# Kernel optimization log

Measured on AMD Instinct MI355X. Metric: run time of the kernel, lower is better.

Reference implementation:

```python
import jax, jax.numpy as jnp
import numpy as np

N = 8192          # num_relations
IN_DIM = 512      # 2 * entity_dim
HID = 256         # hidden_dim
REL_DIM = 256     # relation_dim


def setup_inputs() -> dict:
    key = jax.random.key(0)
    ks = jax.random.split(key, 8)
    s = 1.0 / np.sqrt(IN_DIM)
    return {
        "relation": jax.random.normal(ks[0], (N, REL_DIM), dtype=jnp.float32),
        "context": jax.random.normal(ks[1], (N, IN_DIM), dtype=jnp.float32),
        "adj_tensor": jax.random.randint(ks[2], (N, N), 0, 2).astype(jnp.float32),
        "W_common": jax.random.normal(ks[3], (HID, IN_DIM), dtype=jnp.float32) * s,
        "w_left": jax.random.normal(ks[4], (HID,), dtype=jnp.float32) * (1.0 / np.sqrt(HID)),
        "b_left": jax.random.normal(ks[5], (), dtype=jnp.float32) * 0.01,
        "w_right": jax.random.normal(ks[6], (HID,), dtype=jnp.float32) * (1.0 / np.sqrt(HID)),
        "b_right": jax.random.normal(ks[7], (), dtype=jnp.float32) * 0.01,
    }


def reference(relation, context, adj_tensor, W_common, w_left, b_left, w_right, b_right):
    # common linear (no bias): (N, IN_DIM) @ (IN_DIM, HID) -> (N, HID)
    in_fts = context @ W_common.T
    left = in_fts @ w_left + b_left          # (N,)
    right = in_fts @ w_right + b_right       # (N,)
    logits = left[:, None] + right[None, :]  # additive outer-sum -> (N, N)
    logits = jnp.where(logits >= 0, logits, 0.2 * logits)  # leaky_relu(0.2)
    logits = jnp.where(adj_tensor <= 0.0, -jnp.inf, logits)
    coefs = jax.nn.softmax(logits, axis=-1)  # (N, N)
    x = coefs @ relation                     # (N, REL_DIM)
    return jax.nn.relu(x)
```

## Files before the change

### kernel.cpp

```cpp
#include <hip/hip_runtime.h>

#define NREL 8192
#define RD   256
#define RSHIFT 16.0f

typedef float f32x4 __attribute__((ext_vector_type(4)));
typedef short s16x8 __attribute__((ext_vector_type(8)));
typedef unsigned int  u32;
typedef unsigned short u16;
typedef unsigned long long u64;
typedef u32 u32x4 __attribute__((ext_vector_type(4)));

__device__ __forceinline__ u16 f2bf(float f) {
    u32 b = __float_as_uint(f);
    return (u16)((b + 0x7FFFu + ((b >> 16) & 1u)) >> 16);
}
__device__ __forceinline__ u32 pk_bf16(float lo, float hi) {
    u32 r;
    asm("v_cvt_pk_bf16_f32 %0, %1, %2" : "=v"(r) : "v"(lo), "v"(hi));
    return r;
}

__global__ __launch_bounds__(256) void k_prep_bf(
    const float* __restrict__ W, const float* __restrict__ wl,
    const float* __restrict__ wr, float* __restrict__ ul,
    float* __restrict__ ur, const float* __restrict__ R,
    u32* __restrict__ Bf)
{
    __shared__ float sL[256], sR[256];
    const int t = threadIdx.x;
    if (blockIdx.x < 32) {
        const int d = blockIdx.x * 16 + (t & 15);
        float aL = 0.f, aR = 0.f;
        for (int h = (t >> 4); h < 256; h += 16) {
            float w = W[h * 512 + d];
            aL += w * wl[h];
            aR += w * wr[h];
        }
        sL[t] = aL; sR[t] = aR;
        __syncthreads();
        if (t < 16) {
            float xL = 0.f, xR = 0.f;
            for (int g = 0; g < 16; g++) { xL += sL[g * 16 + t]; xR += sR[g * 16 + t]; }
            ul[blockIdx.x * 16 + t] = xL;
            ur[blockIdx.x * 16 + t] = xR;
        }
        return;
    }
    if (!Bf) return;
    const int b     = blockIdx.x - 32;
    const int jt    = b >> 1;
    const int fbase = (b & 1) * 1024;
    #pragma unroll
    for (int rep = 0; rep < 4; rep++) {
        const int f    = fbase + rep * 256 + t;
        const int kk   = f >> 10;
        const int cg   = (f >> 6) & 15;
        const int lane = f & 63;
        const int lq   = lane >> 4;
        const int l15  = lane & 15;
        const int j0   = (jt << 6) + kk * 32 + lq * 8;
        const int n    = cg * 16 + l15;
        const float* src = R + (size_t)j0 * RD + n;
        float v[8];
        #pragma unroll
        for (int e = 0; e < 8; e++) v[e] = src[(size_t)e * RD];
        u32x4 w;
        w.x = pk_bf16(v[0], v[1]);
        w.y = pk_bf16(v[2], v[3]);
        w.z = pk_bf16(v[4], v[5]);
        w.w = pk_bf16(v[6], v[7]);
        *(u32x4*)(Bf + ((size_t)jt * 2048 + f) * 4) = w;
    }
}

__global__ __launch_bounds__(256) void k_lr(
    const float* __restrict__ ctx, const float* __restrict__ ul,
    const float* __restrict__ ur, const float* __restrict__ bl,
    const float* __restrict__ br, float* __restrict__ left,
    float* __restrict__ right)
{
    const int lane = threadIdx.x & 63;
    const int row  = blockIdx.x * 4 + (threadIdx.x >> 6);
    const f32x4* cv = (const f32x4*)(ctx + (size_t)row * 512);
    const f32x4* uv = (const f32x4*)ul;
    const f32x4* vv = (const f32x4*)ur;
    f32x4 c0 = cv[lane], c1 = cv[lane + 64];
    f32x4 u0 = uv[lane], u1 = uv[lane + 64];
    f32x4 v0 = vv[lane], v1 = vv[lane + 64];
    float dl = c0.x*u0.x + c0.y*u0.y + c0.z*u0.z + c0.w*u0.w
             + c1.x*u1.x + c1.y*u1.y + c1.z*u1.z + c1.w*u1.w;
    float dr = c0.x*v0.x + c0.y*v0.y + c0.z*v0.z + c0.w*v0.w
             + c1.x*v1.x + c1.y*v1.y + c1.z*v1.z + c1.w*v1.w;
    #pragma unroll
    for (int o = 1; o < 64; o <<= 1) { dl += __shfl_xor(dl, o); dr += __shfl_xor(dr, o); }
    if (lane == 0) {
        left[row]  = dl + bl[0];
        right[row] = dr + br[0];
    }
}

template<int S>
__global__ __launch_bounds__(1024) void k_attn_f(
    const float* __restrict__ adj, const s16x8* __restrict__ Bf,
    const float* __restrict__ left, const float* __restrict__ right,
    float* __restrict__ pnum, float* __restrict__ pden)
{
    __shared__ u32 Pl[2][4096];

    const int tid  = threadIdx.x;
    const int lane = tid & 63;
    const int wv   = tid >> 6;
    const int l15  = lane & 15;
    const int lq   = lane >> 4;
    const int rg   = wv >> 3;
    const int cg8  = wv & 7;
    const int s      = (int)(blockIdx.x % (unsigned)S);
    const int rowblk = (int)(blockIdx.x / (unsigned)S) * 128;
    const int jt0 = s * (128 / S);
    const int jt1 = jt0 + (128 / S);

    const int pr = tid >> 4;
    const int pq = tid & 15;

    const float lft0 = left[rowblk + pr];
    const float lft1 = left[rowblk + pr + 64];
    float z;
    z = lft0 + RSHIFT; const float m0 = fmaxf(z, 0.2f * z);
    z = lft1 + RSHIFT; const float m1 = fmaxf(z, 0.2f * z);

    f32x4 acc[4][2];
    #pragma unroll
    for (int i = 0; i < 4; i++) { acc[i][0] = (f32x4)0.f; acc[i][1] = (f32x4)0.f; }
    float dp0 = 0.f, dp1 = 0.f;

    const f32x4* adjv = (const f32x4*)adj;
    const f32x4* rv4  = (const f32x4*)right;
    const size_t arow0 = (size_t)(rowblk + pr) * 2048;
    const size_t arow1 = (size_t)(rowblk + pr + 64) * 2048;

    const u32 widx0 = (u32)pr * 32 + (((u32)pq * 2) ^ (((u32)pr & 7) << 2));
    const u32 widx1 = widx0 + 2048;

    f32x4 aA0 = adjv[arow0 + jt0 * 16 + pq];
    f32x4 aA1 = adjv[arow1 + jt0 * 16 + pq];
    f32x4 rvA = rv4[jt0 * 16 + pq];
    f32x4 aB0 = adjv[arow0 + (jt0 + 1) * 16 + pq];
    f32x4 aB1 = adjv[arow1 + (jt0 + 1) * 16 + pq];
    f32x4 rvB = rv4[(jt0 + 1) * 16 + pq];
    s16x8 bA[2][2], bB[2][2];
    #pragma unroll
    for (int kk = 0; kk < 2; kk++)
        #pragma unroll
        for (int ct = 0; ct < 2; ct++)
            bA[kk][ct] = Bf[(size_t)jt0 * 2048 + kk * 1024 + (cg8 * 2 + ct) * 64 + lane];

    for (int jt = jt0; jt < jt1; jt += 2) {
        {
            float pa[4], pb[4];
            #pragma unroll
            for (int e = 0; e < 4; e++) {
                const float r = rvA[e];
                float z0 = lft0 + r; float s0 = fmaxf(z0, 0.2f * z0);
                pa[e] = aA0[e] * __expf(s0 - m0);
                float z1 = lft1 + r; float s1 = fmaxf(z1, 0.2f * z1);
                pb[e] = aA1[e] * __expf(s1 - m1);
            }
            dp0 += pa[0] + pa[1] + pa[2] + pa[3];
            dp1 += pb[0] + pb[1] + pb[2] + pb[3];
            Pl[0][widx0]     = pk_bf16(pa[0], pa[1]);
            Pl[0][widx0 + 1] = pk_bf16(pa[2], pa[3]);
            Pl[0][widx1]     = pk_bf16(pb[0], pb[1]);
            Pl[0][widx1 + 1] = pk_bf16(pb[2], pb[3]);

            asm volatile("s_waitcnt lgkmcnt(0)" ::: "memory");
            __builtin_amdgcn_s_barrier();

            const int j2 = (jt + 2 < jt1) ? jt + 2 : jt0;
            aA0 = adjv[arow0 + j2 * 16 + pq];
            aA1 = adjv[arow1 + j2 * 16 + pq];
            rvA = rv4[j2 * 16 + pq];
            #pragma unroll
            for (int kk = 0; kk < 2; kk++)
                #pragma unroll
                for (int ct = 0; ct < 2; ct++)
                    bB[kk][ct] = Bf[(size_t)(jt + 1) * 2048 + kk * 1024
                                    + (cg8 * 2 + ct) * 64 + lane];

            const u16* Pu = (const u16*)Pl[0];
            #pragma unroll
            for (int kk = 0; kk < 2; kk++) {
                s16x8 af[4];
                #pragma unroll
                for (int rt = 0; rt < 4; rt++) {
                    const int row = rg * 64 + rt * 16 + l15;
                    const int us  = row * 64 + ((kk * 32 + lq * 8) ^ ((row & 7) << 3));
                    af[rt] = *(const s16x8*)(Pu + us);
                }
                #pragma unroll
                for (int ct = 0; ct < 2; ct++)
                    #pragma unroll
                    for (int rt = 0; rt < 4; rt++)
                        acc[rt][ct] = __builtin_amdgcn_mfma_f32_16x16x32_bf16(
                            af[rt], bA[kk][ct], acc[rt][ct], 0, 0, 0);
            }
        }
        {
            float pa[4], pb[4];
            #pragma unroll
            for (int e = 0; e < 4; e++) {
                const float r = rvB[e];
                float z0 = lft0 + r; float s0 = fmaxf(z0, 0.2f * z0);
                pa[e] = aB0[e] * __expf(s0 - m0);
                float z1 = lft1 + r; float s1 = fmaxf(z1, 0.2f * z1);
                pb[e] = aB1[e] * __expf(s1 - m1);
            }
            dp0 += pa[0] + pa[1] + pa[2] + pa[3];
            dp1 += pb[0] + pb[1] + pb[2] + pb[3];
            Pl[1][widx0]     = pk_bf16(pa[0], pa[1]);
            Pl[1][widx0 + 1] = pk_bf16(pa[2], pa[3]);
            Pl[1][widx1]     = pk_bf16(pb[0], pb[1]);
            Pl[1][widx1 + 1] = pk_bf16(pb[2], pb[3]);

            asm volatile("s_waitcnt lgkmcnt(0)" ::: "memory");
            __builtin_amdgcn_s_barrier();

            const int j3 = (jt + 3 < jt1) ? jt + 3 : jt0;
            aB0 = adjv[arow0 + j3 * 16 + pq];
            aB1 = adjv[arow1 + j3 * 16 + pq];
            rvB = rv4[j3 * 16 + pq];
            const int j2 = (jt + 2 < jt1) ? jt + 2 : jt0;
            #pragma unroll
            for (int kk = 0; kk < 2; kk++)
                #pragma unroll
                for (int ct = 0; ct < 2; ct++)
                    bA[kk][ct] = Bf[(size_t)j2 * 2048 + kk * 1024
                                    + (cg8 * 2 + ct) * 64 + lane];

            const u16* Pu = (const u16*)Pl[1];
            #pragma unroll
            for (int kk = 0; kk < 2; kk++) {
                s16x8 af[4];
                #pragma unroll
                for (int rt = 0; rt < 4; rt++) {
                    const int row = rg * 64 + rt * 16 + l15;
                    const int us  = row * 64 + ((kk * 32 + lq * 8) ^ ((row & 7) << 3));
                    af[rt] = *(const s16x8*)(Pu + us);
                }
                #pragma unroll
                for (int ct = 0; ct < 2; ct++)
                    #pragma unroll
                    for (int rt = 0; rt < 4; rt++)
                        acc[rt][ct] = __builtin_amdgcn_mfma_f32_16x16x32_bf16(
                            af[rt], bB[kk][ct], acc[rt][ct], 0, 0, 0);
            }
        }
    }

    #pragma unroll
    for (int o = 1; o < 16; o <<= 1) { dp0 += __shfl_xor(dp0, o); dp1 += __shfl_xor(dp1, o); }
    if (pq == 0) {
        pden[(size_t)s * NREL + rowblk + pr]      = dp0;
        pden[(size_t)s * NREL + rowblk + pr + 64] = dp1;
    }
    float* pn = pnum + (size_t)s * NREL * RD;
    #pragma unroll
    for (int rt = 0; rt < 4; rt++)
        #pragma unroll
        for (int ct = 0; ct < 2; ct++)
            #pragma unroll
            for (int r = 0; r < 4; r++) {
                const int row = rg * 64 + rt * 16 + lq * 4 + r;
                pn[(size_t)(rowblk + row) * RD + (cg8 * 32 + ct * 16 + l15)] =
                    acc[rt][ct][r];
            }
}

template<int S>
__global__ __launch_bounds__(256) void k_red(
    const float* __restrict__ pnum, const float* __restrict__ pden,
    float* __restrict__ out)
{
    const int idx = blockIdx.x * 256 + threadIdx.x;
    const int row = idx >> 6;
    float den = 0.f;
    #pragma unroll
    for (int s = 0; s < S; s++) den += pden[(size_t)s * NREL + row];
    const f32x4* pn4 = (const f32x4*)pnum;
    f32x4 a = (f32x4)0.f;
    #pragma unroll
    for (int s = 0; s < S; s++) a += pn4[(size_t)s * (NREL * RD / 4) + idx];
    f32x4 r;
    r.x = fmaxf(a.x / den, 0.f);
    r.y = fmaxf(a.y / den, 0.f);
    r.z = fmaxf(a.z / den, 0.f);
    r.w = fmaxf(a.w / den, 0.f);
    ((f32x4*)out)[idx] = r;
}

__global__ __launch_bounds__(512) void k_attn_leg(
    const float* __restrict__ adj, const float* __restrict__ rel,
    const float* __restrict__ left, const float* __restrict__ right,
    float* __restrict__ outp)
{
    __shared__ u32   Pl[64 * 32];
    __shared__ float dnm[64];
    const int tid  = threadIdx.x;
    const int lane = tid & 63;
    const int wv   = tid >> 6;
    const int l15  = lane & 15;
    const int lq   = lane >> 4;
    const int rowblk = blockIdx.x * 64;
    const int pr = tid >> 4, pq = tid & 15;
    const float lft0 = left[rowblk + pr];
    const float lft1 = left[rowblk + pr + 32];
    float z;
    z = lft0 + RSHIFT; const float m0 = fmaxf(z, 0.2f * z);
    z = lft1 + RSHIFT; const float m1 = fmaxf(z, 0.2f * z);
    f32x4 acc[4][2];
    #pragma unroll
    for (int i = 0; i < 4; i++) { acc[i][0] = (f32x4)0.f; acc[i][1] = (f32x4)0.f; }
    float dp0 = 0.f, dp1 = 0.f;
    const f32x4* adjv = (const f32x4*)adj;
    const f32x4* rv4  = (const f32x4*)right;
    const size_t arow0 = (size_t)(rowblk + pr) * 2048;
    const size_t arow1 = (size_t)(rowblk + pr + 32) * 2048;
    const int n0 = wv * 32 + l15;
    const u32 widx0 = (u32)pr * 32 + (((u32)pq * 2) ^ (((u32)pr & 7) << 2));
    const u32 widx1 = widx0 + 1024;
    for (int jb = 0; jb < NREL; jb += 64) {
        f32x4 a0 = adjv[arow0 + (jb >> 2) + pq];
        f32x4 a1 = adjv[arow1 + (jb >> 2) + pq];
        f32x4 rv = rv4[(jb >> 2) + pq];
        s16x8 bc[2][2];
        #pragma unroll
        for (int kk = 0; kk < 2; kk++)
            #pragma unroll
            for (int ct = 0; ct < 2; ct++) {
                const float* rp = rel + (size_t)(jb + kk * 32 + lq * 8) * RD
                                      + (n0 + ct * 16);
                s16x8 b;
                #pragma unroll
                for (int e = 0; e < 8; e++) b[e] = (short)f2bf(rp[(size_t)e * RD]);
                bc[kk][ct] = b;
            }
        float pa[4], pb[4];
        #pragma unroll
        for (int e = 0; e < 4; e++) {
            const float r = rv[e];
            float z0 = lft0 + r; float s0 = fmaxf(z0, 0.2f * z0);
            pa[e] = a0[e] * __expf(s0 - m0);
            float z1 = lft1 + r; float s1 = fmaxf(z1, 0.2f * z1);
            pb[e] = a1[e] * __expf(s1 - m1);
        }
        dp0 += pa[0] + pa[1] + pa[2] + pa[3];
        dp1 += pb[0] + pb[1] + pb[2] + pb[3];
        Pl[widx0]     = pk_bf16(pa[0], pa[1]);
        Pl[widx0 + 1] = pk_bf16(pa[2], pa[3]);
        Pl[widx1]     = pk_bf16(pb[0], pb[1]);
        Pl[widx1 + 1] = pk_bf16(pb[2], pb[3]);
        __syncthreads();
        #pragma unroll
        for (int kk = 0; kk < 2; kk++) {
            s16x8 af[4];
            #pragma unroll
            for (int rt = 0; rt < 4; rt++) {
                const int row = rt * 16 + l15;
                const int us  = row * 64 + ((kk * 32 + lq * 8) ^ ((row & 7) << 3));
                af[rt] = *(const s16x8*)((const u16*)Pl + us);
            }
            #pragma unroll
            for (int ct = 0; ct < 2; ct++)
                #pragma unroll
                for (int rt = 0; rt < 4; rt++)
                    acc[rt][ct] = __builtin_amdgcn_mfma_f32_16x16x32_bf16(
                        af[rt], bc[kk][ct], acc[rt][ct], 0, 0, 0);
        }
        __syncthreads();
    }
    #pragma unroll
    for (int o = 1; o < 16; o <<= 1) { dp0 += __shfl_xor(dp0, o); dp1 += __shfl_xor(dp1, o); }
    if (pq == 0) { dnm[pr] = dp0; dnm[pr + 32] = dp1; }
    __syncthreads();
    #pragma unroll
    for (int rt = 0; rt < 4; rt++)
        #pragma unroll
        for (int ct = 0; ct < 2; ct++)
            #pragma unroll
            for (int r = 0; r < 4; r++) {
                const int row = rt * 16 + lq * 4 + r;
                float v = acc[rt][ct][r] / dnm[row];
                outp[(size_t)(rowblk + row) * RD + (wv * 32 + ct * 16 + l15)] =
                    fmaxf(v, 0.f);
            }
}

extern "C" void kernel_launch(void* const* d_in, const int* in_sizes, int n_in,
                              void* d_out, int out_size, void* d_ws, size_t ws_size,
                              hipStream_t stream)
{
    const float* relation = (const float*)d_in[0];
    const float* context  = (const float*)d_in[1];
    const float* adj      = (const float*)d_in[2];
    const float* W        = (const float*)d_in[3];
    const float* wl       = (const float*)d_in[4];
    const float* bl       = (const float*)d_in[5];
    const float* wr       = (const float*)d_in[6];
    const float* br       = (const float*)d_in[7];
    float* out = (float*)d_out;

    float* wsf   = (float*)d_ws;
    float* ul    = wsf;
    float* ur    = wsf + 512;
    float* left  = wsf + 1024;
    float* right = wsf + 1024 + 8192;
    const size_t hdr  = 81920;
    const size_t bf_b = (size_t)NREL * RD * 2;
    u32* Bf   = (u32*)((char*)d_ws + hdr);
    float* pnum = (float*)((char*)d_ws + hdr + bf_b);

    const int S = 4;
    const size_t need = hdr + bf_b
                      + (size_t)S * NREL * RD * 4 + (size_t)S * NREL * 4;

    if (ws_size >= need) {
        float* pden = pnum + (size_t)S * NREL * RD;
        hipLaunchKernelGGL(k_prep_bf, dim3(288), dim3(256), 0, stream,
                           W, wl, wr, ul, ur, relation, Bf);
        hipLaunchKernelGGL(k_lr, dim3(2048), dim3(256), 0, stream,
                           context, ul, ur, bl, br, left, right);
        hipLaunchKernelGGL((k_attn_f<4>), dim3(64 * 4), dim3(1024), 0, stream,
                           adj, (const s16x8*)Bf, left, right, pnum, pden);
        hipLaunchKernelGGL((k_red<4>), dim3(2048), dim3(256), 0, stream,
                           pnum, pden, out);
    } else {
        hipLaunchKernelGGL(k_prep_bf, dim3(32), dim3(256), 0, stream,
                           W, wl, wr, ul, ur, relation, (u32*)nullptr);
        hipLaunchKernelGGL(k_lr, dim3(2048), dim3(256), 0, stream,
                           context, ul, ur, bl, br, left, right);
        hipLaunchKernelGGL(k_attn_leg, dim3(128), dim3(512), 0, stream,
                           adj, relation, left, right, out);
    }
}
```

Before: 110.4 us.

## Restructure attention kernel to 64-row blocks with 4-tile groups per barrier

The fused attention kernel now uses 512-thread blocks covering 64 rows instead of 1024 threads covering 128, doubling the grid. Each iteration stages four 64-column P tiles in shared memory, with one pair of barriers per group instead of one per tile. Each thread loads 16 contiguous floats of adj per row rather than 4 strided ones. A per-block rotation staggers the starting column group so concurrent blocks read different parts of B. The aim is fewer barriers, wider adjacency loads and better occupancy, at the cost of more registers per thread and B fragments being reused across only 64 rows.

```diff
diff --git a/kernel.cpp b/kernel.cpp
--- a/kernel.cpp
+++ b/kernel.cpp
@@ -101,30 +101,30 @@
 }
 
 template<int S>
-__global__ __launch_bounds__(1024) void k_attn_f(
+__global__ __launch_bounds__(512) void k_attn_f(
     const float* __restrict__ adj, const s16x8* __restrict__ Bf,
     const float* __restrict__ left, const float* __restrict__ right,
     float* __restrict__ pnum, float* __restrict__ pden)
 {
-    __shared__ u32 Pl[2][4096];
+    __shared__ u32 Pt[4 * 2048];
+    constexpr int NT = 128 / S;
+    constexpr int NG = NT / 4;
 
     const int tid  = threadIdx.x;
     const int lane = tid & 63;
     const int wv   = tid >> 6;
     const int l15  = lane & 15;
     const int lq   = lane >> 4;
-    const int rg   = wv >> 3;
-    const int cg8  = wv & 7;
     const int s      = (int)(blockIdx.x % (unsigned)S);
-    const int rowblk = (int)(blockIdx.x / (unsigned)S) * 128;
-    const int jt0 = s * (128 / S);
-    const int jt1 = jt0 + (128 / S);
+    const int rowblk = (int)(blockIdx.x / (unsigned)S) * 64;
+    const int jt0 = s * NT;
+    const int rot = (int)(blockIdx.x & (NG - 1));
 
     const int pr = tid >> 4;
     const int pq = tid & 15;
 
     const float lft0 = left[rowblk + pr];
-    const float lft1 = left[rowblk + pr + 64];
+    const float lft1 = left[rowblk + pr + 32];
     float z;
     z = lft0 + RSHIFT; const float m0 = fmaxf(z, 0.2f * z);
     z = lft1 + RSHIFT; const float m1 = fmaxf(z, 0.2f * z);
@@ -137,131 +137,113 @@
     const f32x4* adjv = (const f32x4*)adj;
     const f32x4* rv4  = (const f32x4*)right;
     const size_t arow0 = (size_t)(rowblk + pr) * 2048;
-    const size_t arow1 = (size_t)(rowblk + pr + 64) * 2048;
-
-    const u32 widx0 = (u32)pr * 32 + (((u32)pq * 2) ^ (((u32)pr & 7) << 2));
-    const u32 widx1 = widx0 + 2048;
-
-    f32x4 aA0 = adjv[arow0 + jt0 * 16 + pq];
-    f32x4 aA1 = adjv[arow1 + jt0 * 16 + pq];
-    f32x4 rvA = rv4[jt0 * 16 + pq];
-    f32x4 aB0 = adjv[arow0 + (jt0 + 1) * 16 + pq];
-    f32x4 aB1 = adjv[arow1 + (jt0 + 1) * 16 + pq];
-    f32x4 rvB = rv4[(jt0 + 1) * 16 + pq];
+    const size_t arow1 = (size_t)(rowblk + pr + 32) * 2048;
+
+    const u32 bc  = (u32)(pq & 3) * 8;
+    const u32 swz = ((u32)pr & 7) << 2;
+    u32* const Pb = Pt + (size_t)(pq >> 2) * 2048;
+
+    #define GBASE(g) (jt0 + (((g) + rot) & (NG - 1)) * 4)
+
+    f32x4 a0[4], a1[4], rr[4];
+    {
+        const int jg = GBASE(0);
+        #pragma unroll
+        for (int q = 0; q < 4; q++) {
+            a0[q] = adjv[arow0 + jg * 16 + pq * 4 + q];
+            a1[q] = adjv[arow1 + jg * 16 + pq * 4 + q];
+            rr[q] = rv4[jg * 16 + pq * 4 + q];
+        }
+    }
     s16x8 bA[2][2], bB[2][2];
     #pragma unroll
     for (int kk = 0; kk < 2; kk++)
         #pragma unroll
         for (int ct = 0; ct < 2; ct++)
-            bA[kk][ct] = Bf[(size_t)jt0 * 2048 + kk * 1024 + (cg8 * 2 + ct) * 64 + lane];
-
-    for (int jt = jt0; jt < jt1; jt += 2) {
-        {
+            bA[kk][ct] = Bf[(size_t)GBASE(0) * 2048 + kk * 1024
+                            + (wv * 2 + ct) * 64 + lane];
+
+    #define BLOAD(DST, JT)                                                     \
+        _Pragma("unroll")                                                      \
+        for (int kk = 0; kk < 2; kk++)                                         \
+            _Pragma("unroll")                                                  \
+            for (int ct = 0; ct < 2; ct++)                                     \
+                DST[kk][ct] = Bf[(size_t)(JT) * 2048 + kk * 1024               \
+                                 + (wv * 2 + ct) * 64 + lane];
+
+    #define MFMA_TILE(TT, BSLOT)                                               \
+        {                                                                      \
+            const u16* Pu = (const u16*)(Pt + (TT) * 2048);                    \
+            _Pragma("unroll")                                                  \
+            for (int kk = 0; kk < 2; kk++) {                                   \
+                s16x8 af[4];                                                   \
+                _Pragma("unroll")                                              \
+                for (int rt = 0; rt < 4; rt++) {                               \
+                    const int row = rt * 16 + l15;                             \
+                    const int us  = row * 64                                   \
+                                  + ((kk * 32 + lq * 8) ^ ((row & 7) << 3));   \
+                    af[rt] = *(const s16x8*)(Pu + us);                         \
+                }                                                              \
+                _Pragma("unroll")                                              \
+                for (int ct = 0; ct < 2; ct++)                                 \
+                    _Pragma("unroll")                                          \
+                    for (int rt = 0; rt < 4; rt++)                             \
+                        acc[rt][ct] = __builtin_amdgcn_mfma_f32_16x16x32_bf16( \
+                            af[rt], BSLOT[kk][ct], acc[rt][ct], 0, 0, 0);      \
+            }                                                                  \
+        }
+
+    for (int g = 0; g < NG; g++) {
+        const int jgc = GBASE(g);
+        const int jgn = GBASE((g + 1 < NG) ? g + 1 : 0);
+
+        #pragma unroll
+        for (int q = 0; q < 4; q++) {
             float pa[4], pb[4];
             #pragma unroll
             for (int e = 0; e < 4; e++) {
-                const float r = rvA[e];
+                const float r = rr[q][e];
                 float z0 = lft0 + r; float s0 = fmaxf(z0, 0.2f * z0);
-                pa[e] = aA0[e] * __expf(s0 - m0);
+                pa[e] = a0[q][e] * __expf(s0 - m0);
                 float z1 = lft1 + r; float s1 = fmaxf(z1, 0.2f * z1);
-                pb[e] = aA1[e] * __expf(s1 - m1);
+                pb[e] = a1[q][e] * __expf(s1 - m1);
             }
             dp0 += pa[0] + pa[1] + pa[2] + pa[3];
             dp1 += pb[0] + pb[1] + pb[2] + pb[3];
-            Pl[0][widx0]     = pk_bf16(pa[0], pa[1]);
-            Pl[0][widx0 + 1] = pk_bf16(pa[2], pa[3]);
-            Pl[0][widx1]     = pk_bf16(pb[0], pb[1]);
-            Pl[0][widx1 + 1] = pk_bf16(pb[2], pb[3]);
-
-            asm volatile("s_waitcnt lgkmcnt(0)" ::: "memory");
-            __builtin_amdgcn_s_barrier();
-
-            const int j2 = (jt + 2 < jt1) ? jt + 2 : jt0;
-            aA0 = adjv[arow0 + j2 * 16 + pq];
-            aA1 = adjv[arow1 + j2 * 16 + pq];
-            rvA = rv4[j2 * 16 + pq];
-            #pragma unroll
-            for (int kk = 0; kk < 2; kk++)
-                #pragma unroll
-                for (int ct = 0; ct < 2; ct++)
-                    bB[kk][ct] = Bf[(size_t)(jt + 1) * 2048 + kk * 1024
-                                    + (cg8 * 2 + ct) * 64 + lane];
-
-            const u16* Pu = (const u16*)Pl[0];
-            #pragma unroll
-            for (int kk = 0; kk < 2; kk++) {
-                s16x8 af[4];
-                #pragma unroll
-                for (int rt = 0; rt < 4; rt++) {
-                    const int row = rg * 64 + rt * 16 + l15;
-                    const int us  = row * 64 + ((kk * 32 + lq * 8) ^ ((row & 7) << 3));
-                    af[rt] = *(const s16x8*)(Pu + us);
-                }
-                #pragma unroll
-                for (int ct = 0; ct < 2; ct++)
-                    #pragma unroll
-                    for (int rt = 0; rt < 4; rt++)
-                        acc[rt][ct] = __builtin_amdgcn_mfma_f32_16x16x32_bf16(
-                            af[rt], bA[kk][ct], acc[rt][ct], 0, 0, 0);
-            }
-        }
-        {
-            float pa[4], pb[4];
-            #pragma unroll
-            for (int e = 0; e < 4; e++) {
-                const float r = rvB[e];
-                float z0 = lft0 + r; float s0 = fmaxf(z0, 0.2f * z0);
-                pa[e] = aB0[e] * __expf(s0 - m0);
-                float z1 = lft1 + r; float s1 = fmaxf(z1, 0.2f * z1);
-                pb[e] = aB1[e] * __expf(s1 - m1);
-            }
-            dp0 += pa[0] + pa[1] + pa[2] + pa[3];
-            dp1 += pb[0] + pb[1] + pb[2] + pb[3];
-            Pl[1][widx0]     = pk_bf16(pa[0], pa[1]);
-            Pl[1][widx0 + 1] = pk_bf16(pa[2], pa[3]);
-            Pl[1][widx1]     = pk_bf16(pb[0], pb[1]);
-            Pl[1][widx1 + 1] = pk_bf16(pb[2], pb[3]);
-
-            asm volatile("s_waitcnt lgkmcnt(0)" ::: "memory");
-            __builtin_amdgcn_s_barrier();
-
-            const int j3 = (jt + 3 < jt1) ? jt + 3 : jt0;
-            aB0 = adjv[arow0 + j3 * 16 + pq];
-            aB1 = adjv[arow1 + j3 * 16 + pq];
-            rvB = rv4[j3 * 16 + pq];
-            const int j2 = (jt + 2 < jt1) ? jt + 2 : jt0;
-            #pragma unroll
-            for (int kk = 0; kk < 2; kk++)
-                #pragma unroll
-                for (int ct = 0; ct < 2; ct++)
-                    bA[kk][ct] = Bf[(size_t)j2 * 2048 + kk * 1024
-                                    + (cg8 * 2 + ct) * 64 + lane];
-
-            const u16* Pu = (const u16*)Pl[1];
-            #pragma unroll
-            for (int kk = 0; kk < 2; kk++) {
-                s16x8 af[4];
-                #pragma unroll
-                for (int rt = 0; rt < 4; rt++) {
-                    const int row = rg * 64 + rt * 16 + l15;
-                    const int us  = row * 64 + ((kk * 32 + lq * 8) ^ ((row & 7) << 3));
-                    af[rt] = *(const s16x8*)(Pu + us);
-                }
-                #pragma unroll
-                for (int ct = 0; ct < 2; ct++)
-                    #pragma unroll
-                    for (int rt = 0; rt < 4; rt++)
-                        acc[rt][ct] = __builtin_amdgcn_mfma_f32_16x16x32_bf16(
-                            af[rt], bB[kk][ct], acc[rt][ct], 0, 0, 0);
-            }
-        }
-    }
+            const u32 i0 = (u32)pr * 32 + ((bc + q * 2) ^ swz);
+            Pb[i0]        = pk_bf16(pa[0], pa[1]);
+            Pb[i0 + 1]    = pk_bf16(pa[2], pa[3]);
+            Pb[i0 + 1024] = pk_bf16(pb[0], pb[1]);
+            Pb[i0 + 1025] = pk_bf16(pb[2], pb[3]);
+        }
+
+        asm volatile("s_waitcnt lgkmcnt(0)" ::: "memory");
+        __builtin_amdgcn_s_barrier();
+
+        #pragma unroll
+        for (int q = 0; q < 4; q++) {
+            a0[q] = adjv[arow0 + jgn * 16 + pq * 4 + q];
+            a1[q] = adjv[arow1 + jgn * 16 + pq * 4 + q];
+            rr[q] = rv4[jgn * 16 + pq * 4 + q];
+        }
+
+        BLOAD(bB, jgc + 1);  MFMA_TILE(0, bA);
+        BLOAD(bA, jgc + 2);  MFMA_TILE(1, bB);
+        BLOAD(bB, jgc + 3);  MFMA_TILE(2, bA);
+        BLOAD(bA, jgn);      MFMA_TILE(3, bB);
+
+        asm volatile("s_waitcnt lgkmcnt(0)" ::: "memory");
+        __builtin_amdgcn_s_barrier();
+    }
+    #undef GBASE
+    #undef BLOAD
+    #undef MFMA_TILE
 
     #pragma unroll
     for (int o = 1; o < 16; o <<= 1) { dp0 += __shfl_xor(dp0, o); dp1 += __shfl_xor(dp1, o); }
     if (pq == 0) {
         pden[(size_t)s * NREL + rowblk + pr]      = dp0;
-        pden[(size_t)s * NREL + rowblk + pr + 64] = dp1;
+        pden[(size_t)s * NREL + rowblk + pr + 32] = dp1;
     }
     float* pn = pnum + (size_t)s * NREL * RD;
     #pragma unroll
@@ -270,8 +252,8 @@
         for (int ct = 0; ct < 2; ct++)
             #pragma unroll
             for (int r = 0; r < 4; r++) {
-                const int row = rg * 64 + rt * 16 + lq * 4 + r;
-                pn[(size_t)(rowblk + row) * RD + (cg8 * 32 + ct * 16 + l15)] =
+                const int row = rt * 16 + lq * 4 + r;
+                pn[(size_t)(rowblk + row) * RD + (wv * 32 + ct * 16 + l15)] =
                     acc[rt][ct][r];
             }
 }
@@ -429,7 +411,7 @@
                            W, wl, wr, ul, ur, relation, Bf);
         hipLaunchKernelGGL(k_lr, dim3(2048), dim3(256), 0, stream,
                            context, ul, ur, bl, br, left, right);
-        hipLaunchKernelGGL((k_attn_f<4>), dim3(64 * 4), dim3(1024), 0, stream,
+        hipLaunchKernelGGL((k_attn_f<4>), dim3(128 * 4), dim3(512), 0, stream,
                            adj, (const s16x8*)Bf, left, right, pnum, pden);
         hipLaunchKernelGGL((k_red<4>), dim3(2048), dim3(256), 0, stream,
                            pnum, pden, out);
```

Measured after the change: 116.3 us. 5.3% more time.
